# Kernel optimization log

Measured on AMD Instinct MI355X. Metric: run time of the kernel, lower is better.

## Reference

```python
import jax, jax.numpy as jnp
import numpy as np

B = 524288

def setup_inputs() -> dict:
    key = jax.random.key(0)
    ks = jax.random.split(key, 9)
    return {
        "x":  jax.random.uniform(ks[0], (B, 1, 9, 9), dtype=jnp.float32),
        "Wc": jax.random.normal(ks[1], (81, 9), dtype=jnp.float32),
        "bc": jax.random.normal(ks[2], (81,), dtype=jnp.float32),
        "Wh": jax.random.normal(ks[3], (27, 9), dtype=jnp.float32),
        "bh": jax.random.normal(ks[4], (27,), dtype=jnp.float32),
        "Wm": jax.random.normal(ks[5], (12, 9), dtype=jnp.float32),
        "bm": jax.random.normal(ks[6], (12,), dtype=jnp.float32),
        "Wo": jax.random.normal(ks[7], (4, 4), dtype=jnp.float32),
        "bo": jax.random.normal(ks[8], (4,), dtype=jnp.float32),
    }

def _forward(x, Wc, bc, Wh, bh, Wm, bm, Wo, bo):
    b = x.shape[0]
    # 9 non-overlapping 3x3 patches (stride 3 over 9x9): (B, 9 patches, 9 pixels)
    p = x[:, 0].reshape(b, 3, 3, 3, 3).transpose(0, 1, 3, 2, 4).reshape(b, 9, 9)
    # conv layer: 9 logic kernels per patch -> (B, 9, 9) -> (B, 81)
    feat = jax.nn.sigmoid(
        jnp.einsum('bgp,gkp->bgk', p, Wc.reshape(9, 9, 9)) + bc.reshape(9, 9)
    ).reshape(b, 81)
    # hidden layer: 9 groups x 3 neurons, each over 9 inputs -> (B, 27)
    h = jax.nn.sigmoid(
        jnp.einsum('bgp,gnp->bgn', feat.reshape(b, 9, 9), Wh.reshape(9, 3, 9))
        + bh.reshape(9, 3)
    ).reshape(b, 27)
    # middle layer: 3 groups x 4 neurons, each over 9 inputs -> (B, 12)
    m = jax.nn.sigmoid(
        jnp.einsum('bgp,gnp->bgn', h.reshape(b, 3, 9), Wm.reshape(3, 4, 9))
        + bm.reshape(3, 4)
    ).reshape(b, 12)
    # output layer: class c reads middle group c % 3 (4 values each)
    num_classes = Wo.shape[0]
    grp = jnp.arange(num_classes) % 3                   # (C,)
    mg = m.reshape(b, 3, 4)[:, grp]                     # (B, C, 4)
    output_logits = jnp.einsum('bcp,cp->bc', mg, Wo) + bo
    return output_logits

def reference(x, Wc, bc, Wh, bh, Wm, bm, Wo, bo):
    return _forward(x, Wc, bc, Wh, bh, Wm, bm, Wo, bo)
```

## Files before the change

kernel.cpp:

```cpp
#include <hip/hip_runtime.h>
#include <stdint.h>

#define THREADS 256
#define WAVE_DW 1792
#define GDW     28

typedef const __attribute__((address_space(1))) uint32_t* gas_ptr;
typedef __attribute__((address_space(3))) uint32_t*       las_ptr;

__device__ __forceinline__ float fast_sigmoid(float v) {
    float e = __expf(-v);
    return __builtin_amdgcn_rcpf(1.0f + e);
}

__global__ __launch_bounds__(THREADS, 4) void olcnn_kernel(
    const float* __restrict__ x,
    const float* __restrict__ Wc, const float* __restrict__ bc,
    const float* __restrict__ Wh, const float* __restrict__ bh,
    const float* __restrict__ Wm, const float* __restrict__ bm,
    const float* __restrict__ Wo, const float* __restrict__ bo,
    float* __restrict__ out)
{
    __shared__ __align__(16) float sm[4 * WAVE_DW];

    const int tid   = threadIdx.x;
    const int lane  = tid & 63;
    const int wid   = tid >> 6;
    const int samp  = blockIdx.x * THREADS + tid;
    const int TOTAL = (int)gridDim.x * THREADS * 81;
    const int LIM   = TOTAL - 4;

    float* smw = sm + wid * WAVE_DW;
    const int wbase81 = (blockIdx.x * THREADS + wid * 64) * 81;

    float res[4];

    #pragma unroll
    for (int G = 0; G < 3; ++G) {
        asm volatile("s_waitcnt lgkmcnt(0)" ::: "memory");
        __builtin_amdgcn_sched_barrier(0);

        {
            int t = (lane * 9363) >> 16;
            int r = lane - t * 7;
            int t81 = t * 81;
            const int gofs = wbase81 + G * 27;
            #pragma unroll
            for (int i = 0; i < 7; ++i) {
                int f0 = gofs + t81 + (r << 2);
                f0 = (f0 < LIM) ? f0 : LIM;
                __builtin_amdgcn_global_load_lds(
                    (gas_ptr)(x + f0), (las_ptr)(smw + i * 256), 16, 0, 0);
                t81 += (r == 6) ? 810 : 729;
                r = (r == 6) ? 0 : r + 1;
            }
        }
        asm volatile("s_waitcnt vmcnt(0)" ::: "memory");

        float p[28];
        {
            const float4* rp = (const float4*)(smw + lane * GDW);
            #pragma unroll
            for (int q = 0; q < 7; ++q) {
                float4 v = rp[q];
                p[4*q+0] = v.x; p[4*q+1] = v.y; p[4*q+2] = v.z; p[4*q+3] = v.w;
            }
        }
        if (G == 2 && samp == (int)gridDim.x * THREADS - 1) {
            p[24] = x[TOTAL - 3]; p[25] = x[TOTAL - 2]; p[26] = x[TOTAL - 1];
        }

        float hbuf[9];
        #pragma unroll
        for (int j = 0; j < 3; ++j) {
            const int g = G * 3 + j;
            float feat[9];
            #pragma unroll
            for (int k = 0; k < 9; ++k) {
                float acc = bc[g * 9 + k];
                #pragma unroll
                for (int pr = 0; pr < 3; ++pr)
                    #pragma unroll
                    for (int pc = 0; pc < 3; ++pc)
                        acc = fmaf(p[pr * 9 + j * 3 + pc],
                                   Wc[(g * 9 + k) * 9 + pr * 3 + pc], acc);
                feat[k] = fast_sigmoid(acc);
            }
            #pragma unroll
            for (int n = 0; n < 3; ++n) {
                float acc = bh[g * 3 + n];
                #pragma unroll
                for (int pi = 0; pi < 9; ++pi)
                    acc = fmaf(feat[pi], Wh[(g * 3 + n) * 9 + pi], acc);
                hbuf[j * 3 + n] = fast_sigmoid(acc);
            }
        }

        float m[4];
        #pragma unroll
        for (int n = 0; n < 4; ++n) {
            float acc = bm[G * 4 + n];
            #pragma unroll
            for (int pi = 0; pi < 9; ++pi)
                acc = fmaf(hbuf[pi], Wm[(G * 4 + n) * 9 + pi], acc);
            m[n] = fast_sigmoid(acc);
        }

        {
            float acc = bo[G];
            #pragma unroll
            for (int pi = 0; pi < 4; ++pi)
                acc = fmaf(m[pi], Wo[G * 4 + pi], acc);
            res[G] = acc;
        }
        if (G == 0) {
            float acc = bo[3];
            #pragma unroll
            for (int pi = 0; pi < 4; ++pi)
                acc = fmaf(m[pi], Wo[3 * 4 + pi], acc);
            res[3] = acc;
        }
    }

    float4 o;
    o.x = res[0]; o.y = res[1]; o.z = res[2]; o.w = res[3];
    ((float4*)out)[samp] = o;
}

extern "C" void kernel_launch(void* const* d_in, const int* in_sizes, int n_in,
                              void* d_out, int out_size, void* d_ws, size_t ws_size,
                              hipStream_t stream) {
    const float* x  = (const float*)d_in[0];
    const float* Wc = (const float*)d_in[1];
    const float* bc = (const float*)d_in[2];
    const float* Wh = (const float*)d_in[3];
    const float* bh = (const float*)d_in[4];
    const float* Wm = (const float*)d_in[5];
    const float* bm = (const float*)d_in[6];
    const float* Wo = (const float*)d_in[7];
    const float* bo = (const float*)d_in[8];
    float* out = (float*)d_out;

    const int B = in_sizes[0] / 81;
    const int blocks = B / THREADS;
    olcnn_kernel<<<blocks, THREADS, 0, stream>>>(x, Wc, bc, Wh, bh, Wm, bm,
                                                 Wo, bo, out);
}
```

Before: 298.4 us.

## Double-buffer LDS staging of input groups to overlap loads with compute

Shrinks blocks to a single 64-lane wave and adds a two-buffer LDS ring. Group 1's global-to-LDS loads are issued before group 0 is computed, and group 2's loads are issued into the freed buffer, with partial vmcnt waits replacing full drains. This is meant to hide global load latency behind the sigmoid/FMA compute within each wave. The cost is a second LDS buffer per wave, smaller blocks and more in-flight loads, which can affect occupancy and scheduling.

```diff
diff --git a/kernel.cpp b/kernel.cpp
--- a/kernel.cpp
+++ b/kernel.cpp
@@ -1,9 +1,8 @@
 #include <hip/hip_runtime.h>
 #include <stdint.h>
 
-#define THREADS 256
-#define WAVE_DW 1792
-#define GDW     28
+#define THREADS 64
+#define BUF_DW  1792
 
 typedef const __attribute__((address_space(1))) uint32_t* gas_ptr;
 typedef __attribute__((address_space(3))) uint32_t*       las_ptr;
@@ -11,6 +10,63 @@
 __device__ __forceinline__ float fast_sigmoid(float v) {
     float e = __expf(-v);
     return __builtin_amdgcn_rcpf(1.0f + e);
+}
+
+template<int G>
+__device__ __forceinline__ void compute_group(
+    const float* __restrict__ p,
+    const float* __restrict__ Wc, const float* __restrict__ bc,
+    const float* __restrict__ Wh, const float* __restrict__ bh,
+    const float* __restrict__ Wm, const float* __restrict__ bm,
+    const float* __restrict__ Wo, const float* __restrict__ bo,
+    float& outA, float& outB)
+{
+    float hb[9];
+    #pragma unroll
+    for (int j = 0; j < 3; ++j) {
+        const int g = G * 3 + j;
+        float feat[9];
+        #pragma unroll
+        for (int k = 0; k < 9; ++k) {
+            float acc = bc[g * 9 + k];
+            #pragma unroll
+            for (int pr = 0; pr < 3; ++pr)
+                #pragma unroll
+                for (int pc = 0; pc < 3; ++pc)
+                    acc = fmaf(p[pr * 9 + j * 3 + pc],
+                               Wc[(g * 9 + k) * 9 + pr * 3 + pc], acc);
+            feat[k] = fast_sigmoid(acc);
+        }
+        #pragma unroll
+        for (int n = 0; n < 3; ++n) {
+            float acc = bh[g * 3 + n];
+            #pragma unroll
+            for (int pi = 0; pi < 9; ++pi)
+                acc = fmaf(feat[pi], Wh[(g * 3 + n) * 9 + pi], acc);
+            hb[j * 3 + n] = fast_sigmoid(acc);
+        }
+    }
+    float m[4];
+    #pragma unroll
+    for (int n = 0; n < 4; ++n) {
+        float acc = bm[G * 4 + n];
+        #pragma unroll
+        for (int pi = 0; pi < 9; ++pi)
+            acc = fmaf(hb[pi], Wm[(G * 4 + n) * 9 + pi], acc);
+        m[n] = fast_sigmoid(acc);
+    }
+    float acc = bo[G];
+    #pragma unroll
+    for (int pi = 0; pi < 4; ++pi)
+        acc = fmaf(m[pi], Wo[G * 4 + pi], acc);
+    outA = acc;
+    if (G == 0) {
+        float acc2 = bo[3];
+        #pragma unroll
+        for (int pi = 0; pi < 4; ++pi)
+            acc2 = fmaf(m[pi], Wo[12 + pi], acc2);
+        outB = acc2;
+    }
 }
 
 __global__ __launch_bounds__(THREADS, 4) void olcnn_kernel(
@@ -21,109 +77,68 @@
     const float* __restrict__ Wo, const float* __restrict__ bo,
     float* __restrict__ out)
 {
-    __shared__ __align__(16) float sm[4 * WAVE_DW];
+    __shared__ __align__(16) float sm[2 * BUF_DW];
 
-    const int tid   = threadIdx.x;
-    const int lane  = tid & 63;
-    const int wid   = tid >> 6;
-    const int samp  = blockIdx.x * THREADS + tid;
+    const int lane  = threadIdx.x;
+    const int samp  = blockIdx.x * THREADS + lane;
     const int TOTAL = (int)gridDim.x * THREADS * 81;
     const int LIM   = TOTAL - 4;
+    const int LAST  = (int)gridDim.x * THREADS - 1;
+    const int wbase81 = blockIdx.x * THREADS * 81;
 
-    float* smw = sm + wid * WAVE_DW;
-    const int wbase81 = (blockIdx.x * THREADS + wid * 64) * 81;
+    const int t0 = (lane * 9363) >> 16;
+    const int r0 = lane - t0 * 7;
 
-    float res[4];
+    auto STAGE = [&](int Ga, float* dst) {
+        int t81 = t0 * 81;
+        int r   = r0;
+        const int gofs = wbase81 + Ga * 27;
+        #pragma unroll
+        for (int i = 0; i < 7; ++i) {
+            int f0 = gofs + t81 + (r << 2);
+            f0 = (f0 < LIM) ? f0 : LIM;
+            __builtin_amdgcn_global_load_lds(
+                (gas_ptr)(x + f0), (las_ptr)(dst + i * 256), 16, 0, 0);
+            t81 += (r == 6) ? 810 : 729;
+            r = (r == 6) ? 0 : r + 1;
+        }
+    };
+    auto READP = [&](const float* buf, float* p) {
+        const float4* rp = (const float4*)(buf + lane * 28);
+        #pragma unroll
+        for (int q = 0; q < 7; ++q) {
+            float4 v = rp[q];
+            p[4*q+0] = v.x; p[4*q+1] = v.y; p[4*q+2] = v.z; p[4*q+3] = v.w;
+        }
+    };
 
-    #pragma unroll
-    for (int G = 0; G < 3; ++G) {
-        asm volatile("s_waitcnt lgkmcnt(0)" ::: "memory");
-        __builtin_amdgcn_sched_barrier(0);
+    float res0, res1, res2, res3;
 
-        {
-            int t = (lane * 9363) >> 16;
-            int r = lane - t * 7;
-            int t81 = t * 81;
-            const int gofs = wbase81 + G * 27;
-            #pragma unroll
-            for (int i = 0; i < 7; ++i) {
-                int f0 = gofs + t81 + (r << 2);
-                f0 = (f0 < LIM) ? f0 : LIM;
-                __builtin_amdgcn_global_load_lds(
-                    (gas_ptr)(x + f0), (las_ptr)(smw + i * 256), 16, 0, 0);
-                t81 += (r == 6) ? 810 : 729;
-                r = (r == 6) ? 0 : r + 1;
-            }
-        }
-        asm volatile("s_waitcnt vmcnt(0)" ::: "memory");
+    STAGE(0, sm);
+    STAGE(1, sm + BUF_DW);
 
-        float p[28];
-        {
-            const float4* rp = (const float4*)(smw + lane * GDW);
-            #pragma unroll
-            for (int q = 0; q < 7; ++q) {
-                float4 v = rp[q];
-                p[4*q+0] = v.x; p[4*q+1] = v.y; p[4*q+2] = v.z; p[4*q+3] = v.w;
-            }
-        }
-        if (G == 2 && samp == (int)gridDim.x * THREADS - 1) {
-            p[24] = x[TOTAL - 3]; p[25] = x[TOTAL - 2]; p[26] = x[TOTAL - 1];
-        }
+    asm volatile("s_waitcnt vmcnt(7)" ::: "memory");
+    float p0[28];
+    READP(sm, p0);
+    asm volatile("s_waitcnt lgkmcnt(0)" ::: "memory");
+    STAGE(2, sm);
+    compute_group<0>(p0, Wc, bc, Wh, bh, Wm, bm, Wo, bo, res0, res3);
 
-        float hbuf[9];
-        #pragma unroll
-        for (int j = 0; j < 3; ++j) {
-            const int g = G * 3 + j;
-            float feat[9];
-            #pragma unroll
-            for (int k = 0; k < 9; ++k) {
-                float acc = bc[g * 9 + k];
-                #pragma unroll
-                for (int pr = 0; pr < 3; ++pr)
-                    #pragma unroll
-                    for (int pc = 0; pc < 3; ++pc)
-                        acc = fmaf(p[pr * 9 + j * 3 + pc],
-                                   Wc[(g * 9 + k) * 9 + pr * 3 + pc], acc);
-                feat[k] = fast_sigmoid(acc);
-            }
-            #pragma unroll
-            for (int n = 0; n < 3; ++n) {
-                float acc = bh[g * 3 + n];
-                #pragma unroll
-                for (int pi = 0; pi < 9; ++pi)
-                    acc = fmaf(feat[pi], Wh[(g * 3 + n) * 9 + pi], acc);
-                hbuf[j * 3 + n] = fast_sigmoid(acc);
-            }
-        }
+    asm volatile("s_waitcnt vmcnt(7)" ::: "memory");
+    float p1[28];
+    READP(sm + BUF_DW, p1);
+    compute_group<1>(p1, Wc, bc, Wh, bh, Wm, bm, Wo, bo, res1, res1);
 
-        float m[4];
-        #pragma unroll
-        for (int n = 0; n < 4; ++n) {
-            float acc = bm[G * 4 + n];
-            #pragma unroll
-            for (int pi = 0; pi < 9; ++pi)
-                acc = fmaf(hbuf[pi], Wm[(G * 4 + n) * 9 + pi], acc);
-            m[n] = fast_sigmoid(acc);
-        }
-
-        {
-            float acc = bo[G];
-            #pragma unroll
-            for (int pi = 0; pi < 4; ++pi)
-                acc = fmaf(m[pi], Wo[G * 4 + pi], acc);
-            res[G] = acc;
-        }
-        if (G == 0) {
-            float acc = bo[3];
-            #pragma unroll
-            for (int pi = 0; pi < 4; ++pi)
-                acc = fmaf(m[pi], Wo[3 * 4 + pi], acc);
-            res[3] = acc;
-        }
+    asm volatile("s_waitcnt vmcnt(0)" ::: "memory");
+    float p2[28];
+    READP(sm, p2);
+    if (samp == LAST) {
+        p2[24] = x[TOTAL - 3]; p2[25] = x[TOTAL - 2]; p2[26] = x[TOTAL - 1];
     }
+    compute_group<2>(p2, Wc, bc, Wh, bh, Wm, bm, Wo, bo, res2, res2);
 
     float4 o;
-    o.x = res[0]; o.y = res[1]; o.z = res[2]; o.w = res[3];
+    o.x = res0; o.y = res1; o.z = res2; o.w = res3;
     ((float4*)out)[samp] = o;
 }
 
```

After: 292.1 us. 1.02x faster.
